# Optimization experiments

Hardware: AMD Instinct MI355X
Metric: run time of the kernel (lower is better)

Reference implementation:

```python
import jax, jax.numpy as jnp
import numpy as np
from jax import lax

D_MODEL = 1024
D_FF = 4096
K = 5
PAD = K // 2


def setup_inputs() -> dict:
    key = jax.random.key(0)
    ks = jax.random.split(key, 12)
    s_in = 1.0 / np.sqrt(D_MODEL)
    s_ff = 1.0 / np.sqrt(D_FF)
    s_k = 1.0 / np.sqrt(K)  # depthwise conv fan_in = 1*K
    return {
        "x": jax.random.normal(ks[0], (4, 2048, D_MODEL), dtype=jnp.float32),
        "Wg": jax.random.uniform(ks[1], (D_MODEL, D_FF), jnp.float32, -s_in, s_in),
        "bg": jax.random.uniform(ks[2], (D_FF,), jnp.float32, -s_in, s_in),
        "Wu": jax.random.uniform(ks[3], (D_MODEL, D_FF), jnp.float32, -s_in, s_in),
        "bu": jax.random.uniform(ks[4], (D_FF,), jnp.float32, -s_in, s_in),
        "convg_w": jax.random.uniform(ks[5], (D_FF, 1, K), jnp.float32, -s_k, s_k),
        "convg_b": jax.random.uniform(ks[6], (D_FF,), jnp.float32, -s_k, s_k),
        "convu_w": jax.random.uniform(ks[7], (D_FF, 1, K), jnp.float32, -s_k, s_k),
        "convu_b": jax.random.uniform(ks[8], (D_FF,), jnp.float32, -s_k, s_k),
        "Wd": jax.random.uniform(ks[9], (D_FF, D_MODEL), jnp.float32, -s_ff, s_ff),
        "bd": jax.random.uniform(ks[10], (D_MODEL,), jnp.float32, -s_ff, s_ff),
    }


def _dwconv(h, w, b):
    # h: [B, L, C] -> depthwise conv along L with 'same' padding -> [B, L, C]
    y = lax.conv_general_dilated(
        h.transpose(0, 2, 1),  # [B, C, L]
        w,                      # [C, 1, K]
        window_strides=(1,),
        padding=[(PAD, PAD)],
        feature_group_count=h.shape[-1],
    )
    return (y + b[None, :, None]).transpose(0, 2, 1)


def reference(x, Wg, bg, Wu, bu, convg_w, convg_b, convu_w, convu_b, Wd, bd):
    gate = _dwconv(jnp.einsum("bld,df->blf", x, Wg) + bg, convg_w, convg_b)
    up = _dwconv(jnp.einsum("bld,df->blf", x, Wu) + bu, convu_w, convu_b)
    h = jax.nn.silu(gate) * up
    return jnp.einsum("blf,fd->bld", h, Wd) + bd
```

## Files before the change

### kernel.cpp

```cpp
#include <hip/hip_runtime.h>
#include <hip/hip_bf16.h>
#include <cstdint>

#define BATCH  4
#define SEQ    2048
#define DMODEL 1024
#define DFF    4096
#define MTOT   (BATCH * SEQ)
#define KCONV  5
#define PADC   2

using bf16raw = unsigned short;
typedef __attribute__((ext_vector_type(8))) short bf16x8;
typedef __attribute__((ext_vector_type(4))) float f32x4;

__device__ __forceinline__ float bf2f(bf16raw u) {
    return __uint_as_float(((uint32_t)u) << 16);
}
__device__ __forceinline__ bf16raw f2bf(float f) {
    uint32_t u = __float_as_uint(f);
    u = (u + 0x7fffu + ((u >> 16) & 1u)) >> 16;
    return (bf16raw)u;
}


__global__ __launch_bounds__(256)
void cvt_bf16_kernel(const float* __restrict__ in, bf16raw* __restrict__ out, int n4)
{
    const int i = blockIdx.x * 256 + threadIdx.x;
    if (i >= n4) return;
    const float4 v = reinterpret_cast<const float4*>(in)[i];
    ushort4 o;
    o.x = f2bf(v.x); o.y = f2bf(v.y); o.z = f2bf(v.z); o.w = f2bf(v.w);
    reinterpret_cast<ushort4*>(out)[i] = o;
}

__global__ __launch_bounds__(256)
void transpose_cvt_kernel(const float* __restrict__ in, bf16raw* __restrict__ out,
                          int R, int C)
{
    __shared__ float tile[32][33];
    const int r0 = blockIdx.y * 32, c0 = blockIdx.x * 32;
    const int tx = threadIdx.x & 31, ty = threadIdx.x >> 5;
#pragma unroll
    for (int i = 0; i < 4; ++i)
        tile[ty + i * 8][tx] = in[(size_t)(r0 + ty + i * 8) * C + c0 + tx];
    __syncthreads();
#pragma unroll
    for (int i = 0; i < 4; ++i)
        out[(size_t)(c0 + ty + i * 8) * R + r0 + tx] = f2bf(tile[tx][ty + i * 8]);
}

__global__ __launch_bounds__(256)
void convw_reorder_kernel(const float* __restrict__ wg, const float* __restrict__ wu,
                          float* __restrict__ wgT, float* __restrict__ wuT)
{
    const int i = blockIdx.x * 256 + threadIdx.x;
    if (i >= KCONV * DFF) return;
    const int j = i / DFF, f = i - j * DFF;
    wgT[i] = wg[f * KCONV + j];
    wuT[i] = wu[f * KCONV + j];
}


__device__ __forceinline__ void gll16(const bf16raw* g, const char* lds)
{
    __builtin_amdgcn_global_load_lds(
        (const __attribute__((address_space(1))) void*)g,
        (__attribute__((address_space(3))) void*)lds, 16, 0, 0);
}

template<typename CT, bool BIAS, int SPLITK, bool COLMAJOR>
__global__ __launch_bounds__(512, 2)
void gemmr_kernel(const bf16raw* __restrict__ A, const bf16raw* __restrict__ BT,
                  const float* __restrict__ bias0, const float* __restrict__ bias1,
                  CT* __restrict__ C, int M, int N, int K, int nbm, int nbn)
{
    __shared__ __align__(16) char smem[131072];

    const int tid  = threadIdx.x;
    const int lane = tid & 63;
    const int wave = __builtin_amdgcn_readfirstlane(tid >> 6);
    const int wr = wave >> 2;
    const int wc = wave & 3;

    const int nwg = nbm * nbn * SPLITK;
    const int cpx = nwg >> 3;
    const int bid = blockIdx.x;
    const int swz = (bid & 7) * cpx + (bid >> 3);
    int sk = 0, rem = swz;
    if constexpr (SPLITK > 1) { sk = swz / (nbm * nbn); rem = swz - sk * (nbm * nbn); }
    int bx, by;
    if constexpr (COLMAJOR) { bx = rem / nbm; by = rem - bx * nbm; }
    else                    { by = rem / nbn; bx = rem - by * nbn; }
    const int bm = by * 256;
    const int bn = bx * 256;

    const int klen = K / SPLITK;
    const int kbeg = sk * klen;
    const int NT   = klen / 32;
    CT* Cp = C + (size_t)sk * M * N;

    const int srow  = tid >> 2;
    const int sphys = tid & 3;

    auto stageA = [&](int t, int half) {
        const int row = half * 128 + srow;
        gll16(A + (size_t)(bm + row) * K + kbeg + t * 32
                + ((sphys ^ ((row >> 1) & 3)) << 3),
              smem + (size_t)(t & 3) * 32768 + row * 64 + sphys * 16);
    };
    auto stageB = [&](int t, int half) {
        const int row = half * 128 + srow;
        gll16(BT + (size_t)(bn + row) * K + kbeg + t * 32
                + ((sphys ^ ((row >> 1) & 3)) << 3),
              smem + (size_t)(t & 3) * 32768 + 16384 + row * 64 + sphys * 16);
    };

    const int g4  = lane >> 4;
    const int r15 = lane & 15;

    auto ldA = [&](int buf, int mf) -> bf16x8 {
        const int row = wr * 128 + mf * 16 + r15;
        return *(const bf16x8*)(smem + (size_t)buf * 32768 + row * 64
                                + ((g4 ^ ((row >> 1) & 3)) << 4));
    };
    auto ldB = [&](int buf, int nf) -> bf16x8 {
        const int row = wc * 64 + nf * 16 + r15;
        return *(const bf16x8*)(smem + (size_t)buf * 32768 + 16384 + row * 64
                                + ((g4 ^ ((row >> 1) & 3)) << 4));
    };

    f32x4 acc[8][4];
#pragma unroll
    for (int i = 0; i < 8; ++i)
#pragma unroll
        for (int j = 0; j < 4; ++j) acc[i][j] = (f32x4){0.f, 0.f, 0.f, 0.f};

    stageA(0, 0); stageA(0, 1); stageB(0, 0); stageB(0, 1);
    stageA(1, 0); stageA(1, 1); stageB(1, 0); stageB(1, 1);

    for (int t = 0; t < NT; ++t) {
        const int buf = t & 3;
        if (t < NT - 1) asm volatile("s_waitcnt vmcnt(4)" ::: "memory");
        else            asm volatile("s_waitcnt vmcnt(0)" ::: "memory");
        __builtin_amdgcn_s_barrier();
        asm volatile("" ::: "memory");

        if (t + 2 < NT) { stageA(t + 2, 0); stageA(t + 2, 1); }
        bf16x8 bfr[4];
#pragma unroll
        for (int nf = 0; nf < 4; ++nf) bfr[nf] = ldB(buf, nf);
        {
            bf16x8 afr[4];
#pragma unroll
            for (int i = 0; i < 4; ++i) afr[i] = ldA(buf, i);
            __builtin_amdgcn_s_setprio(1);
#pragma unroll
            for (int i = 0; i < 4; ++i)
#pragma unroll
                for (int nf = 0; nf < 4; ++nf)
                    acc[i][nf] = __builtin_amdgcn_mfma_f32_16x16x32_bf16(
                        afr[i], bfr[nf], acc[i][nf], 0, 0, 0);
            __builtin_amdgcn_s_setprio(0);
        }

        if (t + 2 < NT) { stageB(t + 2, 0); stageB(t + 2, 1); }
        {
            bf16x8 afr[4];
#pragma unroll
            for (int i = 0; i < 4; ++i) afr[i] = ldA(buf, 4 + i);
            __builtin_amdgcn_s_setprio(1);
#pragma unroll
            for (int i = 0; i < 4; ++i)
#pragma unroll
                for (int nf = 0; nf < 4; ++nf)
                    acc[4 + i][nf] = __builtin_amdgcn_mfma_f32_16x16x32_bf16(
                        afr[i], bfr[nf], acc[4 + i][nf], 0, 0, 0);
            __builtin_amdgcn_s_setprio(0);
        }
        asm volatile("" ::: "memory");
    }

    const int er = g4 << 2;
#pragma unroll
    for (int nf = 0; nf < 4; ++nf) {
        const int nn = bn + wc * 64 + nf * 16 + r15;
        float bv = 0.f;
        if constexpr (BIAS) bv = (nn < DFF) ? bias0[nn] : bias1[nn - DFF];
#pragma unroll
        for (int mf = 0; mf < 8; ++mf) {
            const int mrow = bm + wr * 128 + mf * 16 + er;
#pragma unroll
            for (int j = 0; j < 4; ++j) {
                const float v = acc[mf][nf][j] + bv;
                if constexpr (sizeof(CT) == 2)
                    Cp[(size_t)(mrow + j) * N + nn] = f2bf(v);
                else
                    Cp[(size_t)(mrow + j) * N + nn] = v;
            }
        }
    }
}

template<int NS>
__global__ __launch_bounds__(256)
void reduce_bias_kernel(const float* __restrict__ part, const float* __restrict__ bd,
                        float* __restrict__ out)
{
    const int i = blockIdx.x * 256 + threadIdx.x;
    const int d = (i & (DMODEL / 4 - 1)) * 4;
    const float4 bb = *reinterpret_cast<const float4*>(bd + d);
    float4 o; o.x = bb.x; o.y = bb.y; o.z = bb.z; o.w = bb.w;
#pragma unroll
    for (int s = 0; s < NS; ++s) {
        const float4 a = reinterpret_cast<const float4*>(part + (size_t)s * MTOT * DMODEL)[i];
        o.x += a.x; o.y += a.y; o.z += a.z; o.w += a.w;
    }
    reinterpret_cast<float4*>(out)[i] = o;
}

__global__ __launch_bounds__(256)
void conv_silu_mul_bf16_kernel(const bf16raw* __restrict__ gp, const bf16raw* __restrict__ up,
                               const float* __restrict__ wgT, const float* __restrict__ cbg,
                               const float* __restrict__ wuT, const float* __restrict__ cbu,
                               bf16raw* __restrict__ h, int S)
{
    const int idx = blockIdx.x * 256 + threadIdx.x;
    const int f   = (idx & (DFF / 8 - 1)) << 3;
    const int row = idx >> 9;
    const int l   = row & (SEQ - 1);
    const int rb  = row - l;

    float g[8], u[8];
    {
        const float4 a0 = *reinterpret_cast<const float4*>(cbg + f);
        const float4 a1 = *reinterpret_cast<const float4*>(cbg + f + 4);
        const float4 b0 = *reinterpret_cast<const float4*>(cbu + f);
        const float4 b1 = *reinterpret_cast<const float4*>(cbu + f + 4);
        g[0]=a0.x; g[1]=a0.y; g[2]=a0.z; g[3]=a0.w; g[4]=a1.x; g[5]=a1.y; g[6]=a1.z; g[7]=a1.w;
        u[0]=b0.x; u[1]=b0.y; u[2]=b0.z; u[3]=b0.w; u[4]=b1.x; u[5]=b1.y; u[6]=b1.z; u[7]=b1.w;
    }

#pragma unroll
    for (int j = 0; j < KCONV; ++j) {
        const int ls = l + j - PADC;
        if (ls < 0 || ls >= SEQ) continue;
        const size_t off = (size_t)(rb + ls) * S + f;
        const bf16x8 gv = *reinterpret_cast<const bf16x8*>(gp + off);
        const bf16x8 uv = *reinterpret_cast<const bf16x8*>(up + off);
        const float4 wa0 = *reinterpret_cast<const float4*>(wgT + j * DFF + f);
        const float4 wa1 = *reinterpret_cast<const float4*>(wgT + j * DFF + f + 4);
        const float4 wb0 = *reinterpret_cast<const float4*>(wuT + j * DFF + f);
        const float4 wb1 = *reinterpret_cast<const float4*>(wuT + j * DFF + f + 4);
        const float wg8[8] = {wa0.x, wa0.y, wa0.z, wa0.w, wa1.x, wa1.y, wa1.z, wa1.w};
        const float wu8[8] = {wb0.x, wb0.y, wb0.z, wb0.w, wb1.x, wb1.y, wb1.z, wb1.w};
#pragma unroll
        for (int c = 0; c < 8; ++c) {
            g[c] += bf2f((bf16raw)gv[c]) * wg8[c];
            u[c] += bf2f((bf16raw)uv[c]) * wu8[c];
        }
    }

    bf16x8 hv;
#pragma unroll
    for (int c = 0; c < 8; ++c) {
        const float s = g[c] / (1.f + __expf(-g[c]));
        hv[c] = (short)f2bf(s * u[c]);
    }
    *reinterpret_cast<bf16x8*>(h + (size_t)row * DFF + f) = hv;
}


#define BM 128
#define BN 128
#define BK 8

__device__ __forceinline__ void load4f(const float* p, float v[4]) {
    const float4 t = *reinterpret_cast<const float4*>(p);
    v[0] = t.x; v[1] = t.y; v[2] = t.z; v[3] = t.w;
}

__global__ __launch_bounds__(256)
void sgemm_bias_kernel(const float* __restrict__ A, const float* __restrict__ B,
                       const float* __restrict__ bias, float* __restrict__ C,
                       int N, int K)
{
    __shared__ float As[BK][BM];
    __shared__ float Bs[BK][BN];

    const int tid = threadIdx.x;
    const int bm  = blockIdx.y * BM;
    const int bn  = blockIdx.x * BN;
    const int tx  = tid & 15;
    const int ty  = tid >> 4;

    const int arow = tid >> 1;
    const int acol = (tid & 1) * 4;
    const int brow = tid >> 5;
    const int bcol = (tid & 31) * 4;

    const float* Ap = A + (size_t)(bm + arow) * K + acol;
    const float* Bp = B + (size_t)brow * N + bn + bcol;

    float acc[8][8];
#pragma unroll
    for (int i = 0; i < 8; ++i)
#pragma unroll
        for (int j = 0; j < 8; ++j) acc[i][j] = 0.f;

    for (int k0 = 0; k0 < K; k0 += BK) {
        float av[4];
        load4f(Ap + k0, av);
        const float4 bv = *reinterpret_cast<const float4*>(Bp + (size_t)k0 * N);
        __syncthreads();
#pragma unroll
        for (int i = 0; i < 4; ++i) As[acol + i][arow] = av[i];
        *reinterpret_cast<float4*>(&Bs[brow][bcol]) = bv;
        __syncthreads();
#pragma unroll
        for (int kk = 0; kk < BK; ++kk) {
            const float4 a0 = *reinterpret_cast<const float4*>(&As[kk][ty * 4]);
            const float4 a1 = *reinterpret_cast<const float4*>(&As[kk][64 + ty * 4]);
            const float4 b0 = *reinterpret_cast<const float4*>(&Bs[kk][tx * 4]);
            const float4 b1 = *reinterpret_cast<const float4*>(&Bs[kk][64 + tx * 4]);
            const float am[8] = {a0.x, a0.y, a0.z, a0.w, a1.x, a1.y, a1.z, a1.w};
            const float bb[8] = {b0.x, b0.y, b0.z, b0.w, b1.x, b1.y, b1.z, b1.w};
#pragma unroll
            for (int mi = 0; mi < 8; ++mi)
#pragma unroll
                for (int nj = 0; nj < 8; ++nj)
                    acc[mi][nj] += am[mi] * bb[nj];
        }
    }
#pragma unroll
    for (int mi = 0; mi < 8; ++mi) {
        const int m = bm + ((mi < 4) ? (ty * 4 + mi) : (64 + ty * 4 + (mi - 4)));
#pragma unroll
        for (int g = 0; g < 2; ++g) {
            const int n = bn + g * 64 + tx * 4;
            float4 o;
            o.x = acc[mi][g * 4 + 0] + bias[n + 0];
            o.y = acc[mi][g * 4 + 1] + bias[n + 1];
            o.z = acc[mi][g * 4 + 2] + bias[n + 2];
            o.w = acc[mi][g * 4 + 3] + bias[n + 3];
            *reinterpret_cast<float4*>(&C[(size_t)m * N + n]) = o;
        }
    }
}

__global__ __launch_bounds__(256)
void conv_silu_mul_f32_kernel(const float* __restrict__ gp, const float* __restrict__ up,
                              const float* __restrict__ wg, const float* __restrict__ cbg,
                              const float* __restrict__ wu, const float* __restrict__ cbu,
                              float* __restrict__ hout)
{
    const int idx = blockIdx.x * 256 + threadIdx.x;
    const int f   = (idx & (DFF / 4 - 1)) * 4;
    const int l   = idx >> 10;

    float g[4], u[4];
    load4f(cbg + f, g);
    load4f(cbu + f, u);
#pragma unroll
    for (int j = 0; j < KCONV; ++j) {
        const int ls = l + j - PADC;
        if (ls < 0 || ls >= SEQ) continue;
        const size_t off = (size_t)ls * DFF + f;
        float gv[4], uv[4];
        load4f(gp + off, gv);
        load4f(up + off, uv);
#pragma unroll
        for (int c = 0; c < 4; ++c) {
            g[c] += gv[c] * wg[(f + c) * KCONV + j];
            u[c] += uv[c] * wu[(f + c) * KCONV + j];
        }
    }
    float h[4];
#pragma unroll
    for (int c = 0; c < 4; ++c) {
        const float s = g[c] / (1.f + __expf(-g[c]));
        h[c] = s * u[c];
    }
    float4 o; o.x = h[0]; o.y = h[1]; o.z = h[2]; o.w = h[3];
    *reinterpret_cast<float4*>(&hout[(size_t)l * DFF + f]) = o;
}


extern "C" void kernel_launch(void* const* d_in, const int* in_sizes, int n_in,
                              void* d_out, int out_size, void* d_ws, size_t ws_size,
                              hipStream_t stream)
{
    const float* x   = (const float*)d_in[0];
    const float* Wg  = (const float*)d_in[1];
    const float* bg  = (const float*)d_in[2];
    const float* Wu  = (const float*)d_in[3];
    const float* bu  = (const float*)d_in[4];
    const float* cgw = (const float*)d_in[5];
    const float* cgb = (const float*)d_in[6];
    const float* cuw = (const float*)d_in[7];
    const float* cub = (const float*)d_in[8];
    const float* Wd  = (const float*)d_in[9];
    const float* bd  = (const float*)d_in[10];
    float* out = (float*)d_out;

    const dim3 blk(256);
    auto align256 = [](size_t v) { return (v + 255) & ~(size_t)255; };

    const size_t SZ_XB  = (size_t)MTOT * DMODEL * 2;
    const size_t SZ_WGU = (size_t)2 * DFF * DMODEL * 2;
    const size_t SZ_WD  = (size_t)DMODEL * DFF * 2;
    const size_t SZ_CW  = (size_t)KCONV * DFF * 4;
    const size_t SZ_H   = (size_t)MTOT * DFF * 2;
    const size_t SZ_UP  = (size_t)MTOT * 2 * DFF * 2;

    size_t cur = 0;
    const size_t oXB  = cur; cur = align256(cur + SZ_XB);
    const size_t oWGU = cur; cur = align256(cur + SZ_WGU);
    const size_t oWD  = cur; cur = align256(cur + SZ_WD);
    const size_t oCWg = cur; cur = align256(cur + SZ_CW);
    const size_t oCWu = cur; cur = align256(cur + SZ_CW);
    const size_t oH   = cur; cur = align256(cur + SZ_H);
    const size_t oUP  = cur; cur = align256(cur + SZ_UP);
    const size_t need = cur;

    if (ws_size >= need) {
        bf16raw* xb   = (bf16raw*)((char*)d_ws + oXB);
        bf16raw* Wgu  = (bf16raw*)((char*)d_ws + oWGU);
        bf16raw* WdT  = (bf16raw*)((char*)d_ws + oWD);
        float*   cwg  = (float*)((char*)d_ws + oCWg);
        float*   cwu  = (float*)((char*)d_ws + oCWu);
        bf16raw* h    = (bf16raw*)((char*)d_ws + oH);
        bf16raw* Cup  = (bf16raw*)((char*)d_ws + oUP);
        float*   part = (float*)((char*)d_ws + oUP);

        cvt_bf16_kernel<<<(MTOT * DMODEL / 4 + 255) / 256, blk, 0, stream>>>(x, xb, MTOT * DMODEL / 4);
        transpose_cvt_kernel<<<dim3(DFF / 32, DMODEL / 32), blk, 0, stream>>>(Wg, Wgu, DMODEL, DFF);
        transpose_cvt_kernel<<<dim3(DFF / 32, DMODEL / 32), blk, 0, stream>>>(Wu, Wgu + (size_t)DFF * DMODEL, DMODEL, DFF);
        transpose_cvt_kernel<<<dim3(DMODEL / 32, DFF / 32), blk, 0, stream>>>(Wd, WdT, DFF, DMODEL);
        convw_reorder_kernel<<<(KCONV * DFF + 255) / 256, blk, 0, stream>>>(cgw, cuw, cwg, cwu);

        {
            const int nbm = MTOT / 256, nbn = (2 * DFF) / 256;
            gemmr_kernel<bf16raw, true, 1, true><<<nbm * nbn, dim3(512), 0, stream>>>(
                xb, Wgu, bg, bu, Cup, MTOT, 2 * DFF, DMODEL, nbm, nbn);
        }

        conv_silu_mul_bf16_kernel<<<MTOT * (DFF / 8) / 256, blk, 0, stream>>>(
            Cup, Cup + DFF, cwg, cgb, cwu, cub, h, 2 * DFF);

        {
            const int nbm = MTOT / 256, nbn = DMODEL / 256;
            gemmr_kernel<float, false, 2, false><<<nbm * nbn * 2, dim3(512), 0, stream>>>(
                h, WdT, nullptr, nullptr, part, MTOT, DMODEL, DFF, nbm, nbn);
        }
        reduce_bias_kernel<2><<<MTOT * DMODEL / 4 / 256, blk, 0, stream>>>(part, bd, out);
        return;
    }

    const size_t CE  = (size_t)SEQ * DFF;
    const size_t P32 = CE * sizeof(float);
    if (ws_size < 3 * P32) return;

    float* gpre = (float*)d_ws;
    float* upre = gpre + CE;
    float* hbuf = upre + CE;
    dim3 gu(DFF / BN, SEQ / BM);
    dim3 gdc(DMODEL / BN, SEQ / BM);
    const int nconv = SEQ * (DFF / 4) / 256;
    for (int b = 0; b < BATCH; ++b) {
        const float* xbp = x + (size_t)b * SEQ * DMODEL;
        float* outb = out + (size_t)b * SEQ * DMODEL;
        sgemm_bias_kernel<<<gu, blk, 0, stream>>>(xbp, Wg, bg, gpre, DFF, DMODEL);
        sgemm_bias_kernel<<<gu, blk, 0, stream>>>(xbp, Wu, bu, upre, DFF, DMODEL);
        conv_silu_mul_f32_kernel<<<nconv, blk, 0, stream>>>(gpre, upre, cgw, cgb, cuw, cub, hbuf);
        sgemm_bias_kernel<<<gdc, blk, 0, stream>>>(hbuf, Wd, bd, outb, DMODEL, DFF);
    }
}
```

Before: 388.2 us.

## Software-pipeline LDS fragment loads and deepen global prefetch in GEMM mainloop

Restructures the GEMM main loop so LDS fragment reads for the next A/B slices are issued while MFMAs on the current slices run, using ping-pong register sets for A and B. Global-to-LDS prefetch is deepened from two tiles ahead to three within the four-buffer ring, with the barrier moved late in each iteration. The swizzle offset is now computed once per lane instead of per load. The aim is to hide LDS latency and barrier stalls behind MFMA work, at the cost of more live registers and tighter buffer-reuse timing.

Result: no change. 391.5 us (+0.9%).

```diff
diff --git a/kernel.cpp b/kernel.cpp
--- a/kernel.cpp
+++ b/kernel.cpp
@@ -72,7 +72,7 @@
 
 template<typename CT, bool BIAS, int SPLITK, bool COLMAJOR>
 __global__ __launch_bounds__(512, 2)
-void gemmr_kernel(const bf16raw* __restrict__ A, const bf16raw* __restrict__ BT,
+void gemmp_kernel(const bf16raw* __restrict__ A, const bf16raw* __restrict__ BT,
                   const float* __restrict__ bias0, const float* __restrict__ bias1,
                   CT* __restrict__ C, int M, int N, int K, int nbm, int nbn)
 {
@@ -104,31 +104,34 @@
     const int srow  = tid >> 2;
     const int sphys = tid & 3;
 
-    auto stageA = [&](int t, int half) {
-        const int row = half * 128 + srow;
-        gll16(A + (size_t)(bm + row) * K + kbeg + t * 32
-                + ((sphys ^ ((row >> 1) & 3)) << 3),
-              smem + (size_t)(t & 3) * 32768 + row * 64 + sphys * 16);
+    auto stage = [&](int t) {
+#pragma unroll
+        for (int half = 0; half < 2; ++half) {
+            const int row = half * 128 + srow;
+            gll16(A + (size_t)(bm + row) * K + kbeg + t * 32
+                    + ((sphys ^ ((row >> 1) & 3)) << 3),
+                  smem + (size_t)(t & 3) * 32768 + row * 64 + sphys * 16);
+        }
+#pragma unroll
+        for (int half = 0; half < 2; ++half) {
+            const int row = half * 128 + srow;
+            gll16(BT + (size_t)(bn + row) * K + kbeg + t * 32
+                    + ((sphys ^ ((row >> 1) & 3)) << 3),
+                  smem + (size_t)(t & 3) * 32768 + 16384 + row * 64 + sphys * 16);
+        }
     };
-    auto stageB = [&](int t, int half) {
-        const int row = half * 128 + srow;
-        gll16(BT + (size_t)(bn + row) * K + kbeg + t * 32
-                + ((sphys ^ ((row >> 1) & 3)) << 3),
-              smem + (size_t)(t & 3) * 32768 + 16384 + row * 64 + sphys * 16);
-    };
-
-    const int g4  = lane >> 4;
-    const int r15 = lane & 15;
+
+    const int g4   = lane >> 4;
+    const int r15  = lane & 15;
+    const int koff = ((g4 ^ ((r15 >> 1) & 3)) << 4);
 
     auto ldA = [&](int buf, int mf) -> bf16x8 {
-        const int row = wr * 128 + mf * 16 + r15;
-        return *(const bf16x8*)(smem + (size_t)buf * 32768 + row * 64
-                                + ((g4 ^ ((row >> 1) & 3)) << 4));
+        return *(const bf16x8*)(smem + (size_t)buf * 32768
+                                + (wr * 128 + mf * 16 + r15) * 64 + koff);
     };
     auto ldB = [&](int buf, int nf) -> bf16x8 {
-        const int row = wc * 64 + nf * 16 + r15;
-        return *(const bf16x8*)(smem + (size_t)buf * 32768 + 16384 + row * 64
-                                + ((g4 ^ ((row >> 1) & 3)) << 4));
+        return *(const bf16x8*)(smem + (size_t)buf * 32768 + 16384
+                                + (wc * 64 + nf * 16 + r15) * 64 + koff);
     };
 
     f32x4 acc[8][4];
@@ -137,50 +140,65 @@
 #pragma unroll
         for (int j = 0; j < 4; ++j) acc[i][j] = (f32x4){0.f, 0.f, 0.f, 0.f};
 
-    stageA(0, 0); stageA(0, 1); stageB(0, 0); stageB(0, 1);
-    stageA(1, 0); stageA(1, 1); stageB(1, 0); stageB(1, 1);
-
-    for (int t = 0; t < NT; ++t) {
-        const int buf = t & 3;
-        if (t < NT - 1) asm volatile("s_waitcnt vmcnt(4)" ::: "memory");
-        else            asm volatile("s_waitcnt vmcnt(0)" ::: "memory");
-        __builtin_amdgcn_s_barrier();
-        asm volatile("" ::: "memory");
-
-        if (t + 2 < NT) { stageA(t + 2, 0); stageA(t + 2, 1); }
-        bf16x8 bfr[4];
-#pragma unroll
-        for (int nf = 0; nf < 4; ++nf) bfr[nf] = ldB(buf, nf);
-        {
-            bf16x8 afr[4];
-#pragma unroll
-            for (int i = 0; i < 4; ++i) afr[i] = ldA(buf, i);
-            __builtin_amdgcn_s_setprio(1);
-#pragma unroll
-            for (int i = 0; i < 4; ++i)
-#pragma unroll
-                for (int nf = 0; nf < 4; ++nf)
-                    acc[i][nf] = __builtin_amdgcn_mfma_f32_16x16x32_bf16(
-                        afr[i], bfr[nf], acc[i][nf], 0, 0, 0);
-            __builtin_amdgcn_s_setprio(0);
-        }
-
-        if (t + 2 < NT) { stageB(t + 2, 0); stageB(t + 2, 1); }
-        {
-            bf16x8 afr[4];
-#pragma unroll
-            for (int i = 0; i < 4; ++i) afr[i] = ldA(buf, 4 + i);
-            __builtin_amdgcn_s_setprio(1);
-#pragma unroll
-            for (int i = 0; i < 4; ++i)
-#pragma unroll
-                for (int nf = 0; nf < 4; ++nf)
-                    acc[4 + i][nf] = __builtin_amdgcn_mfma_f32_16x16x32_bf16(
-                        afr[i], bfr[nf], acc[4 + i][nf], 0, 0, 0);
-            __builtin_amdgcn_s_setprio(0);
-        }
-        asm volatile("" ::: "memory");
-    }
+    bf16x8 A0[2], A1[2], Bb0[4], Bb1[4];
+
+#define MFMA_SET(M0, ASET, BSET)                                               \
+    __builtin_amdgcn_s_setprio(1);                                             \
+    _Pragma("unroll")                                                          \
+    for (int i_ = 0; i_ < 2; ++i_)                                             \
+        _Pragma("unroll")                                                      \
+        for (int nf_ = 0; nf_ < 4; ++nf_)                                      \
+            acc[(M0) + i_][nf_] = __builtin_amdgcn_mfma_f32_16x16x32_bf16(     \
+                ASET[i_], BSET[nf_], acc[(M0) + i_][nf_], 0, 0, 0);            \
+    __builtin_amdgcn_s_setprio(0);
+
+#define TILE_BODY(T, BC, BN)                                                   \
+    {                                                                          \
+        const int t_   = (T);                                                  \
+        const int buf_ = t_ & 3;                                               \
+                                 \
+        A1[0] = ldA(buf_, 2); A1[1] = ldA(buf_, 3);                            \
+        MFMA_SET(0, A0, BC)                                                    \
+                                 \
+        A0[0] = ldA(buf_, 4); A0[1] = ldA(buf_, 5);                            \
+        MFMA_SET(2, A1, BC)                                                    \
+                                 \
+        A1[0] = ldA(buf_, 6); A1[1] = ldA(buf_, 7);                            \
+        MFMA_SET(4, A0, BC)                                                    \
+                     \
+        if (t_ + 2 < NT) asm volatile("s_waitcnt vmcnt(4)" ::: "memory");      \
+        else             asm volatile("s_waitcnt vmcnt(0)" ::: "memory");      \
+        __builtin_amdgcn_s_barrier();                                          \
+        asm volatile("" ::: "memory");                                         \
+        if (t_ + 3 < NT) stage(t_ + 3);                                        \
+                       \
+        if (t_ + 1 < NT) {                                                     \
+            const int nb_ = (t_ + 1) & 3;                                      \
+            BN[0] = ldB(nb_, 0); BN[1] = ldB(nb_, 1);                          \
+            BN[2] = ldB(nb_, 2); BN[3] = ldB(nb_, 3);                          \
+            A0[0] = ldA(nb_, 0); A0[1] = ldA(nb_, 1);                          \
+        }                                                                      \
+        MFMA_SET(6, A1, BC)                                                    \
+        asm volatile("" ::: "memory");                                         \
+    }
+
+    stage(0);
+    if (NT > 1) stage(1);
+    if (NT > 2) stage(2);
+    if (NT > 2)      asm volatile("s_waitcnt vmcnt(8)" ::: "memory");
+    else if (NT > 1) asm volatile("s_waitcnt vmcnt(4)" ::: "memory");
+    else             asm volatile("s_waitcnt vmcnt(0)" ::: "memory");
+    __builtin_amdgcn_s_barrier();
+    asm volatile("" ::: "memory");
+    Bb0[0] = ldB(0, 0); Bb0[1] = ldB(0, 1); Bb0[2] = ldB(0, 2); Bb0[3] = ldB(0, 3);
+    A0[0]  = ldA(0, 0); A0[1]  = ldA(0, 1);
+
+    for (int tt = 0; tt < NT; tt += 2) {
+        TILE_BODY(tt, Bb0, Bb1)
+        if (tt + 1 < NT) TILE_BODY(tt + 1, Bb1, Bb0)
+    }
+#undef TILE_BODY
+#undef MFMA_SET
 
     const int er = g4 << 2;
 #pragma unroll
@@ -442,7 +460,7 @@
 
         {
             const int nbm = MTOT / 256, nbn = (2 * DFF) / 256;
-            gemmr_kernel<bf16raw, true, 1, true><<<nbm * nbn, dim3(512), 0, stream>>>(
+            gemmp_kernel<bf16raw, true, 1, true><<<nbm * nbn, dim3(512), 0, stream>>>(
                 xb, Wgu, bg, bu, Cup, MTOT, 2 * DFF, DMODEL, nbm, nbn);
         }
 
@@ -451,7 +469,7 @@
 
         {
             const int nbm = MTOT / 256, nbn = DMODEL / 256;
-            gemmr_kernel<float, false, 2, false><<<nbm * nbn * 2, dim3(512), 0, stream>>>(
+            gemmp_kernel<float, false, 2, false><<<nbm * nbn * 2, dim3(512), 0, stream>>>(
                 h, WdT, nullptr, nullptr, part, MTOT, DMODEL, DFF, nbm, nbn);
         }
         reduce_bias_kernel<2><<<MTOT * DMODEL / 4 / 256, blk, 0, stream>>>(part, bd, out);
```
